# Kernel tuning notes

Hardware: AMD Instinct MI355X
Metric: run time of the kernel (lower is better)

## Reference

```python
import jax, jax.numpy as jnp
import numpy as np
from jax import lax

B, H, W = 512, 128, 128
ARCH = [1, 4096, 4096, 4096, 4096]
CONV_THRESH = 0.0
GRAPH_THRESH = 0.8
EMBED_DIM = 1


def setup_inputs() -> dict:
    key = jax.random.key(0)
    ks = jax.random.split(key, 16)
    inp = {
        "x": jax.random.normal(ks[0], (B, 1, H, W), dtype=jnp.float32),
        "conv_w": jax.random.normal(ks[1], (1, 1, 2, 2), dtype=jnp.float32) * 0.5,
        "conv_b": jax.random.normal(ks[2], (1,), dtype=jnp.float32) * 0.1,
        "rotation": jax.random.normal(ks[3], (EMBED_DIM, EMBED_DIM), dtype=jnp.float32),
        "entangle": jax.random.normal(ks[4], (EMBED_DIM, EMBED_DIM), dtype=jnp.float32),
    }
    # Linear params, torch convention W: [out_f, in_f]
    for i, (fi, fo) in enumerate(zip(ARCH[:-1], ARCH[1:])):
        inp[f"W{i+1}"] = jax.random.normal(ks[5 + 2 * i], (fo, fi), dtype=jnp.float32) / np.sqrt(fi)
        inp[f"b{i+1}"] = jax.random.normal(ks[6 + 2 * i], (fo,), dtype=jnp.float32) * 0.01
    return inp


def _forward(x, conv_w, conv_b, rotation, entangle, W1, b1, W2, b2, W3, b3, W4, b4):
    # ConvFilter: 2x2 valid conv, sigmoid(logits - thresh), mean over C,H,W -> [B]
    logits = lax.conv_general_dilated(
        x, conv_w, window_strides=(1, 1), padding="VALID",
        dimension_numbers=("NCHW", "OIHW", "NCHW"))
    logits = logits + conv_b.reshape(1, -1, 1, 1)
    conv_out = jax.nn.sigmoid(logits - CONV_THRESH).mean(axis=(1, 2, 3))  # [B]
    conv_vec = conv_out[:, None]  # [B, 1] -> embed_dim forced to 1

    # ClassicalSelfAttention (embed_dim = 1)
    q = conv_vec @ rotation                      # [B, 1]
    k = conv_vec @ entangle                      # [B, 1]
    scores = jax.nn.softmax((q @ k.T) / np.sqrt(EMBED_DIM).astype(np.float32), axis=-1)  # [B, B]
    attn_out = scores @ conv_vec                 # [B, 1]

    # tanh MLP stack
    out = attn_out
    acts = []
    for Wl, bl in ((W1, b1), (W2, b2), (W3, b3), (W4, b4)):
        out = jnp.tanh(out @ Wl.T + bl)          # [B, out_f]
        acts.append(out)

    # Vectorized fidelity adjacency over equal-shaped layer activations:
    # normalized Gram matrix squared, thresholded (replaces the O(L^2)
    # Python loop with .item() syncs in the source).
    S = jnp.stack([a.reshape(-1) for a in acts])                  # [L, B*4096]
    S_hat = S / (jnp.linalg.norm(S, axis=1, keepdims=True) + 1e-12)
    fid = (S_hat @ S_hat.T) ** 2                                   # [L, L]
    L = len(acts)
    weights = jnp.where(fid >= GRAPH_THRESH, 1.0, 0.0) * (1.0 - jnp.eye(L, dtype=fid.dtype))
    return out, weights


def reference(x, conv_w, conv_b, rotation, entangle, W1, b1, W2, b2, W3, b3, W4, b4):
    return _forward(x, conv_w, conv_b, rotation, entangle, W1, b1, W2, b2, W3, b3, W4, b4)
```

## Files before the change

kernel.cpp:

```cpp
#include <hip/hip_runtime.h>
#include <cmath>


#define NEL (512 * 4096)

typedef float  floatx4 __attribute__((ext_vector_type(4)));
typedef _Float16 halfx8 __attribute__((ext_vector_type(8)));
typedef _Float16 halfx4 __attribute__((ext_vector_type(4)));

__global__ __launch_bounds__(256) void conv_mean_kernel(
    const float* __restrict__ x, const float* __restrict__ cw,
    const float* __restrict__ cb, float* __restrict__ c_out)
{
  __shared__ float sbuf[4];
  const int b = blockIdx.x;
  const float w00 = cw[0], w01 = cw[1], w10 = cw[2], w11 = cw[3];
  const float bias = cb[0];
  const float* xb = x + (size_t)b * 128 * 128;
  float acc = 0.f;
  for (int t = threadIdx.x; t < 127 * 32; t += 256) {
    const int i  = t >> 5;
    const int j0 = (t & 31) << 2;
    const float* pr0 = xb + i * 128 + j0;
    const float* pr1 = pr0 + 128;
    const float4 a4 = *reinterpret_cast<const float4*>(pr0);
    const float  a5 = pr0[4];
    const float4 b4 = *reinterpret_cast<const float4*>(pr1);
    const float  b5 = pr1[4];
    const float a[5] = {a4.x, a4.y, a4.z, a4.w, a5};
    const float bb[5] = {b4.x, b4.y, b4.z, b4.w, b5};
    #pragma unroll
    for (int m = 0; m < 4; ++m) {
      if (j0 + m < 127) {
        float v = w00 * a[m] + w01 * a[m + 1] + w10 * bb[m] + w11 * bb[m + 1] + bias;
        acc += 1.0f / (1.0f + __expf(-v));
      }
    }
  }
  #pragma unroll
  for (int off = 32; off > 0; off >>= 1) acc += __shfl_down(acc, off, 64);
  const int lane = threadIdx.x & 63, wv = threadIdx.x >> 6;
  if (lane == 0) sbuf[wv] = acc;
  __syncthreads();
  if (threadIdx.x == 0)
    c_out[b] = (sbuf[0] + sbuf[1] + sbuf[2] + sbuf[3]) * (1.0f / 16129.0f);
}

__global__ __launch_bounds__(64) void attn_kernel(
    const float* __restrict__ c, const float* __restrict__ rot,
    const float* __restrict__ ent, float* __restrict__ attn)
{
  const int i = blockIdx.x;
  const int lane = threadIdx.x;
  const float t = rot[0] * ent[0] * c[i];
  float vals[8], cj[8];
  float mx = -1e30f;
  #pragma unroll
  for (int u = 0; u < 8; ++u) {
    float cv = c[lane + u * 64];
    cj[u] = cv;
    vals[u] = t * cv;
    mx = fmaxf(mx, vals[u]);
  }
  #pragma unroll
  for (int off = 32; off > 0; off >>= 1) mx = fmaxf(mx, __shfl_down(mx, off, 64));
  mx = __shfl(mx, 0, 64);
  float se = 0.f, sw = 0.f;
  #pragma unroll
  for (int u = 0; u < 8; ++u) {
    float e = __expf(vals[u] - mx);
    se += e;
    sw += e * cj[u];
  }
  #pragma unroll
  for (int off = 32; off > 0; off >>= 1) {
    se += __shfl_down(se, off, 64);
    sw += __shfl_down(sw, off, 64);
  }
  if (lane == 0) attn[i] = sw / se;
}

__global__ __launch_bounds__(256) void layer1_kernel(
    const float* __restrict__ attn, const float* __restrict__ W1,
    const float* __restrict__ b1, float* __restrict__ act1,
    _Float16* __restrict__ act1h)
{
  const int o = blockIdx.x * 256 + threadIdx.x;
  const int i = blockIdx.y;
  const float v = tanhf(attn[i] * W1[o] + b1[o]);
  act1[(size_t)i * 4096 + o] = v;
  if (act1h) act1h[(size_t)i * 4096 + o] = (_Float16)v;
}

#define BM 128
#define BN 128
#define BK 32
#define LDK 40

template<bool AHALF, bool FUSE>
__global__ __launch_bounds__(256, 4) void gemm_tanh_kernel(
    const void* __restrict__ Av, const float* __restrict__ W,
    const float* __restrict__ bias, float* __restrict__ C)
{
  __shared__ _Float16 As[2][BM][LDK];
  __shared__ _Float16 Ws[2][BN][LDK];
  const int K = 4096, N = 4096;
  const int tid  = threadIdx.x;
  const int lane = tid & 63;
  const int wave = tid >> 6;
  const int wm = (wave >> 1) * 64;
  const int wn = (wave & 1) * 64;
  const int q  = lane >> 4;
  const int ml = lane & 15;
  const int tileM = blockIdx.y * BM;
  const int tileN = blockIdx.x * BN;
  const int Kslice = K / gridDim.z;
  const int kbeg = blockIdx.z * Kslice;
  const int kend = kbeg + Kslice;
  float* Cb = FUSE ? C : C + (size_t)blockIdx.z * NEL;

  floatx4 acc[4][4] = {};

  const int rw  = tid >> 2;
  const int cw0 = (tid & 3) << 3;
  const int ra = tid >> 1;
  const int ca = (tid & 1) << 4;

  float4 pw[4];
  halfx8 pah[2];
  float4 paf[4];

  auto load_tile = [&](int k0) {
    if (AHALF) {
      const _Float16* Ah = (const _Float16*)Av;
      const _Float16* ap = Ah + (size_t)(tileM + ra) * K + k0 + ca;
      pah[0] = *reinterpret_cast<const halfx8*>(ap);
      pah[1] = *reinterpret_cast<const halfx8*>(ap + 8);
    } else {
      const float* Af = (const float*)Av;
      #pragma unroll
      for (int u = 0; u < 2; ++u) {
        const float* ap = Af + (size_t)(tileM + rw + u * 64) * K + k0 + cw0;
        paf[2 * u]     = *reinterpret_cast<const float4*>(ap);
        paf[2 * u + 1] = *reinterpret_cast<const float4*>(ap + 4);
      }
    }
    #pragma unroll
    for (int u = 0; u < 2; ++u) {
      const float* wp = W + (size_t)(tileN + rw + u * 64) * K + k0 + cw0;
      pw[2 * u]     = *reinterpret_cast<const float4*>(wp);
      pw[2 * u + 1] = *reinterpret_cast<const float4*>(wp + 4);
    }
  };
  auto store_tile = [&](int buf) {
    if (AHALF) {
      *reinterpret_cast<halfx8*>(&As[buf][ra][ca])     = pah[0];
      *reinterpret_cast<halfx8*>(&As[buf][ra][ca + 8]) = pah[1];
    } else {
      #pragma unroll
      for (int u = 0; u < 2; ++u) {
        halfx8 ha = { (_Float16)paf[2*u].x, (_Float16)paf[2*u].y,
                      (_Float16)paf[2*u].z, (_Float16)paf[2*u].w,
                      (_Float16)paf[2*u+1].x, (_Float16)paf[2*u+1].y,
                      (_Float16)paf[2*u+1].z, (_Float16)paf[2*u+1].w };
        *reinterpret_cast<halfx8*>(&As[buf][rw + u * 64][cw0]) = ha;
      }
    }
    #pragma unroll
    for (int u = 0; u < 2; ++u) {
      halfx8 hw = { (_Float16)pw[2*u].x, (_Float16)pw[2*u].y,
                    (_Float16)pw[2*u].z, (_Float16)pw[2*u].w,
                    (_Float16)pw[2*u+1].x, (_Float16)pw[2*u+1].y,
                    (_Float16)pw[2*u+1].z, (_Float16)pw[2*u+1].w };
      *reinterpret_cast<halfx8*>(&Ws[buf][rw + u * 64][cw0]) = hw;
    }
  };

  load_tile(kbeg);
  store_tile(0);
  int cur = 0;

  for (int k0 = kbeg; k0 < kend; k0 += BK) {
    const bool more = (k0 + BK < kend);
    __syncthreads();
    if (more) load_tile(k0 + BK);

    halfx8 af[4], bf[4];
    #pragma unroll
    for (int i = 0; i < 4; ++i)
      af[i] = *reinterpret_cast<const halfx8*>(&As[cur][wm + i * 16 + ml][q * 8]);
    #pragma unroll
    for (int j = 0; j < 4; ++j)
      bf[j] = *reinterpret_cast<const halfx8*>(&Ws[cur][wn + j * 16 + ml][q * 8]);

    #pragma unroll
    for (int i = 0; i < 4; ++i)
      #pragma unroll
      for (int j = 0; j < 4; ++j)
        acc[i][j] = __builtin_amdgcn_mfma_f32_16x16x32_f16(af[i], bf[j], acc[i][j], 0, 0, 0);

    if (more) store_tile(cur ^ 1);
    cur ^= 1;
  }

  #pragma unroll
  for (int i = 0; i < 4; ++i) {
    const int row0 = tileM + wm + i * 16 + q * 4;
    #pragma unroll
    for (int j = 0; j < 4; ++j) {
      const int col = tileN + wn + j * 16 + ml;
      if (FUSE) {
        const float bv = bias[col];
        #pragma unroll
        for (int r = 0; r < 4; ++r)
          Cb[(size_t)(row0 + r) * N + col] = tanhf(acc[i][j][r] + bv);
      } else {
        #pragma unroll
        for (int r = 0; r < 4; ++r)
          Cb[(size_t)(row0 + r) * N + col] = acc[i][j][r];
      }
    }
  }
}

template<int S, bool WRITEH>
__global__ __launch_bounds__(256) void combine_tanh_kernel(
    const float* __restrict__ part, const float* __restrict__ bias,
    float* __restrict__ outp, _Float16* __restrict__ outh)
{
  const int i4 = blockIdx.x * 256 + threadIdx.x;
  const floatx4* p4 = (const floatx4*)part;
  floatx4 s = p4[i4];
  #pragma unroll
  for (int z = 1; z < S; ++z) s += p4[(size_t)z * (NEL / 4) + i4];
  const floatx4 bv = ((const floatx4*)bias)[i4 & 1023];
  floatx4 o;
  #pragma unroll
  for (int r = 0; r < 4; ++r) o[r] = tanhf(s[r] + bv[r]);
  ((floatx4*)outp)[i4] = o;
  if (WRITEH) {
    halfx4 h = { (_Float16)o[0], (_Float16)o[1], (_Float16)o[2], (_Float16)o[3] };
    ((halfx4*)outh)[i4] = h;
  }
}

__global__ __launch_bounds__(256) void fid_dots_kernel(
    const float* __restrict__ a1, const float* __restrict__ a2,
    const float* __restrict__ a3, const float* __restrict__ a4,
    float* __restrict__ D)
{
  __shared__ float sred[4][10];
  float s[10] = {0, 0, 0, 0, 0, 0, 0, 0, 0, 0};
  const int n4 = NEL / 4;
  const int stride = gridDim.x * blockDim.x;
  const floatx4* p1 = (const floatx4*)a1;
  const floatx4* p2 = (const floatx4*)a2;
  const floatx4* p3 = (const floatx4*)a3;
  const floatx4* p4 = (const floatx4*)a4;
  for (int i = blockIdx.x * 256 + threadIdx.x; i < n4; i += stride) {
    floatx4 v1 = p1[i], v2 = p2[i], v3 = p3[i], v4 = p4[i];
    #pragma unroll
    for (int r = 0; r < 4; ++r) {
      s[0] += v1[r] * v1[r]; s[1] += v1[r] * v2[r]; s[2] += v1[r] * v3[r];
      s[3] += v1[r] * v4[r]; s[4] += v2[r] * v2[r]; s[5] += v2[r] * v3[r];
      s[6] += v2[r] * v4[r]; s[7] += v3[r] * v3[r]; s[8] += v3[r] * v4[r];
      s[9] += v4[r] * v4[r];
    }
  }
  const int lane = threadIdx.x & 63, wv = threadIdx.x >> 6;
  #pragma unroll
  for (int p = 0; p < 10; ++p) {
    float v = s[p];
    #pragma unroll
    for (int off = 32; off > 0; off >>= 1) v += __shfl_down(v, off, 64);
    if (lane == 0) sred[wv][p] = v;
  }
  __syncthreads();
  if (threadIdx.x < 10) {
    float v = sred[0][threadIdx.x] + sred[1][threadIdx.x] +
              sred[2][threadIdx.x] + sred[3][threadIdx.x];
    atomicAdd(&D[threadIdx.x * 16], v);
  }
}

__global__ void finalize_kernel(const float* __restrict__ D, float* __restrict__ wout)
{
  const int i = threadIdx.x;
  if (i >= 16) return;
  const int p = i >> 2, qq = i & 3;
  const int a = p < qq ? p : qq;
  const int b = p < qq ? qq : p;
  const int base[4] = {0, 4, 7, 9};
  const float dpq = D[(base[a] + (b - a)) * 16];
  const float npv = sqrtf(D[base[p] * 16]) + 1e-12f;
  const float nqv = sqrtf(D[base[qq] * 16]) + 1e-12f;
  const float ch = dpq / (npv * nqv);
  const float fid = ch * ch;
  wout[i] = (fid >= 0.8f && p != qq) ? 1.0f : 0.0f;
}

extern "C" void kernel_launch(void* const* d_in, const int* in_sizes, int n_in,
                              void* d_out, int out_size, void* d_ws, size_t ws_size,
                              hipStream_t stream)
{
  const float* x   = (const float*)d_in[0];
  const float* cw  = (const float*)d_in[1];
  const float* cb  = (const float*)d_in[2];
  const float* rot = (const float*)d_in[3];
  const float* ent = (const float*)d_in[4];
  const float* W1  = (const float*)d_in[5];
  const float* b1  = (const float*)d_in[6];
  const float* W2  = (const float*)d_in[7];
  const float* b2  = (const float*)d_in[8];
  const float* W3  = (const float*)d_in[9];
  const float* b3  = (const float*)d_in[10];
  const float* W4  = (const float*)d_in[11];
  const float* b4  = (const float*)d_in[12];
  float* out = (float*)d_out;

  char*  ws    = (char*)d_ws;
  float* c_buf = (float*)(ws + 0);
  float* attn  = (float*)(ws + 2048);
  float* D     = (float*)(ws + 4096);
  float* act1  = (float*)(ws + 8192);
  float* act2  = act1 + NEL;
  float* act3  = act2 + NEL;
  float* part  = act3 + NEL;
  _Float16* act1h = (_Float16*)(part + (size_t)8 * NEL);
  _Float16* act2h = act1h + NEL;
  _Float16* act3h = act2h + NEL;
  float* wout  = out + NEL;

  const size_t base_need = 8192 + (size_t)3 * NEL * 4;
  const bool sk8h = ws_size >= base_need + (size_t)8 * NEL * 4 + (size_t)3 * NEL * 2;
  const bool sk8  = ws_size >= base_need + (size_t)8 * NEL * 4;

  hipMemsetAsync(D, 0, 10 * 16 * sizeof(float), stream);
  conv_mean_kernel<<<512, 256, 0, stream>>>(x, cw, cb, c_buf);
  attn_kernel<<<512, 64, 0, stream>>>(c_buf, rot, ent, attn);
  layer1_kernel<<<dim3(16, 512), 256, 0, stream>>>(attn, W1, b1, act1,
                                                   sk8h ? act1h : nullptr);

  const int cgrid = NEL / 4 / 256;
  dim3 g8(4096 / BN, 512 / BM, 8);
  if (sk8h) {
    gemm_tanh_kernel<true,false><<<g8, 256, 0, stream>>>(act1h, W2, nullptr, part);
    combine_tanh_kernel<8,true><<<cgrid, 256, 0, stream>>>(part, b2, act2, act2h);
    gemm_tanh_kernel<true,false><<<g8, 256, 0, stream>>>(act2h, W3, nullptr, part);
    combine_tanh_kernel<8,true><<<cgrid, 256, 0, stream>>>(part, b3, act3, act3h);
    gemm_tanh_kernel<true,false><<<g8, 256, 0, stream>>>(act3h, W4, nullptr, part);
    combine_tanh_kernel<8,false><<<cgrid, 256, 0, stream>>>(part, b4, out, nullptr);
  } else if (sk8) {
    gemm_tanh_kernel<false,false><<<g8, 256, 0, stream>>>(act1, W2, nullptr, part);
    combine_tanh_kernel<8,false><<<cgrid, 256, 0, stream>>>(part, b2, act2, nullptr);
    gemm_tanh_kernel<false,false><<<g8, 256, 0, stream>>>(act2, W3, nullptr, part);
    combine_tanh_kernel<8,false><<<cgrid, 256, 0, stream>>>(part, b3, act3, nullptr);
    gemm_tanh_kernel<false,false><<<g8, 256, 0, stream>>>(act3, W4, nullptr, part);
    combine_tanh_kernel<8,false><<<cgrid, 256, 0, stream>>>(part, b4, out, nullptr);
  } else {
    dim3 g1(4096 / BN, 512 / BM, 1);
    gemm_tanh_kernel<false,true><<<g1, 256, 0, stream>>>(act1, W2, b2, act2);
    gemm_tanh_kernel<false,true><<<g1, 256, 0, stream>>>(act2, W3, b3, act3);
    gemm_tanh_kernel<false,true><<<g1, 256, 0, stream>>>(act3, W4, b4, out);
  }

  fid_dots_kernel<<<256, 256, 0, stream>>>(act1, act2, act3, out, D);
  finalize_kernel<<<1, 64, 0, stream>>>(D, wout);
}
```

Before: 434.8 us.

## Drop LDS staging in split-K GEMM, load MFMA fragments directly from global

The GEMM no longer stages tiles in shared memory. Each wave loads its own A and W fragments straight from global memory into registers, prefetching the next W slice one step ahead, and there are no __syncthreads barriers. The grid becomes 1-D with z placed as the fastest index, so the eight K-slices of one output tile are adjacent, and occupancy is lowered to 3 blocks per SM. This removes LDS traffic and barrier cost but drops cross-wave reuse: each W and A element is now fetched by two waves, which raises global and L2 traffic. The fidelity-dot kernel grid is also doubled.

```diff
diff --git a/kernel.cpp b/kernel.cpp
--- a/kernel.cpp
+++ b/kernel.cpp
@@ -92,115 +92,83 @@
   if (act1h) act1h[(size_t)i * 4096 + o] = (_Float16)v;
 }
 
-#define BM 128
-#define BN 128
-#define BK 32
-#define LDK 40
-
 template<bool AHALF, bool FUSE>
-__global__ __launch_bounds__(256, 4) void gemm_tanh_kernel(
+__global__ __launch_bounds__(256, 3) void gemm_sk_kernel(
     const void* __restrict__ Av, const float* __restrict__ W,
-    const float* __restrict__ bias, float* __restrict__ C)
-{
-  __shared__ _Float16 As[2][BM][LDK];
-  __shared__ _Float16 Ws[2][BN][LDK];
+    const float* __restrict__ bias, float* __restrict__ outp)
+{
   const int K = 4096, N = 4096;
-  const int tid  = threadIdx.x;
-  const int lane = tid & 63;
-  const int wave = tid >> 6;
-  const int wm = (wave >> 1) * 64;
-  const int wn = (wave & 1) * 64;
-  const int q  = lane >> 4;
-  const int ml = lane & 15;
-  const int tileM = blockIdx.y * BM;
-  const int tileN = blockIdx.x * BN;
-  const int Kslice = K / gridDim.z;
-  const int kbeg = blockIdx.z * Kslice;
-  const int kend = kbeg + Kslice;
-  float* Cb = FUSE ? C : C + (size_t)blockIdx.z * NEL;
+  const int id = blockIdx.x;
+  int y, x, z, kbeg, kend;
+  if (FUSE) { y = id >> 5; x = id & 31; z = 0; kbeg = 0; kend = K; }
+  else      { y = id >> 8; x = (id >> 3) & 31; z = id & 7;
+              kbeg = z * 512; kend = kbeg + 512; }
+  const int tid = threadIdx.x, lane = tid & 63, wave = tid >> 6;
+  const int wm = (wave >> 1) * 64, wn = (wave & 1) * 64;
+  const int q = lane >> 4, ml = lane & 15;
+  const int tileM = y * 128, tileN = x * 128;
+  float* Cb = FUSE ? outp : outp + (size_t)z * NEL;
+
+  const float* wRow = W + (size_t)(tileN + wn + ml) * K + q * 8;
 
   floatx4 acc[4][4] = {};
-
-  const int rw  = tid >> 2;
-  const int cw0 = (tid & 3) << 3;
-  const int ra = tid >> 1;
-  const int ca = (tid & 1) << 4;
-
-  float4 pw[4];
-  halfx8 pah[2];
-  float4 paf[4];
-
-  auto load_tile = [&](int k0) {
+  halfx8 af[4], wf[4];
+  float4 wr[8];
+
+  auto loadW = [&](float4* d, int k0) {
+    #pragma unroll
+    for (int j = 0; j < 4; ++j) {
+      const float* p = wRow + (size_t)j * 16 * K + k0;
+      d[2 * j]     = *reinterpret_cast<const float4*>(p);
+      d[2 * j + 1] = *reinterpret_cast<const float4*>(p + 4);
+    }
+  };
+  auto cvtW = [&](halfx8* h, const float4* r) {
+    #pragma unroll
+    for (int j = 0; j < 4; ++j)
+      h[j] = halfx8{ (_Float16)r[2*j].x,   (_Float16)r[2*j].y,
+                     (_Float16)r[2*j].z,   (_Float16)r[2*j].w,
+                     (_Float16)r[2*j+1].x, (_Float16)r[2*j+1].y,
+                     (_Float16)r[2*j+1].z, (_Float16)r[2*j+1].w };
+  };
+
+  const _Float16* aRowH = nullptr;
+  const float*    aRowF = nullptr;
+  if (AHALF) aRowH = (const _Float16*)Av + (size_t)(tileM + wm + ml) * K + q * 8;
+  else       aRowF = (const float*)Av    + (size_t)(tileM + wm + ml) * K + q * 8;
+
+  auto loadA = [&](halfx8* d, int k0) {
     if (AHALF) {
-      const _Float16* Ah = (const _Float16*)Av;
-      const _Float16* ap = Ah + (size_t)(tileM + ra) * K + k0 + ca;
-      pah[0] = *reinterpret_cast<const halfx8*>(ap);
-      pah[1] = *reinterpret_cast<const halfx8*>(ap + 8);
-    } else {
-      const float* Af = (const float*)Av;
       #pragma unroll
-      for (int u = 0; u < 2; ++u) {
-        const float* ap = Af + (size_t)(tileM + rw + u * 64) * K + k0 + cw0;
-        paf[2 * u]     = *reinterpret_cast<const float4*>(ap);
-        paf[2 * u + 1] = *reinterpret_cast<const float4*>(ap + 4);
-      }
-    }
-    #pragma unroll
-    for (int u = 0; u < 2; ++u) {
-      const float* wp = W + (size_t)(tileN + rw + u * 64) * K + k0 + cw0;
-      pw[2 * u]     = *reinterpret_cast<const float4*>(wp);
-      pw[2 * u + 1] = *reinterpret_cast<const float4*>(wp + 4);
-    }
-  };
-  auto store_tile = [&](int buf) {
-    if (AHALF) {
-      *reinterpret_cast<halfx8*>(&As[buf][ra][ca])     = pah[0];
-      *reinterpret_cast<halfx8*>(&As[buf][ra][ca + 8]) = pah[1];
+      for (int i = 0; i < 4; ++i)
+        d[i] = *reinterpret_cast<const halfx8*>(aRowH + (size_t)i * 16 * K + k0);
     } else {
       #pragma unroll
-      for (int u = 0; u < 2; ++u) {
-        halfx8 ha = { (_Float16)paf[2*u].x, (_Float16)paf[2*u].y,
-                      (_Float16)paf[2*u].z, (_Float16)paf[2*u].w,
-                      (_Float16)paf[2*u+1].x, (_Float16)paf[2*u+1].y,
-                      (_Float16)paf[2*u+1].z, (_Float16)paf[2*u+1].w };
-        *reinterpret_cast<halfx8*>(&As[buf][rw + u * 64][cw0]) = ha;
+      for (int i = 0; i < 4; ++i) {
+        const float* p = aRowF + (size_t)i * 16 * K + k0;
+        const float4 r0 = *reinterpret_cast<const float4*>(p);
+        const float4 r1 = *reinterpret_cast<const float4*>(p + 4);
+        d[i] = halfx8{ (_Float16)r0.x, (_Float16)r0.y, (_Float16)r0.z, (_Float16)r0.w,
+                       (_Float16)r1.x, (_Float16)r1.y, (_Float16)r1.z, (_Float16)r1.w };
       }
     }
-    #pragma unroll
-    for (int u = 0; u < 2; ++u) {
-      halfx8 hw = { (_Float16)pw[2*u].x, (_Float16)pw[2*u].y,
-                    (_Float16)pw[2*u].z, (_Float16)pw[2*u].w,
-                    (_Float16)pw[2*u+1].x, (_Float16)pw[2*u+1].y,
-                    (_Float16)pw[2*u+1].z, (_Float16)pw[2*u+1].w };
-      *reinterpret_cast<halfx8*>(&Ws[buf][rw + u * 64][cw0]) = hw;
-    }
   };
 
-  load_tile(kbeg);
-  store_tile(0);
-  int cur = 0;
-
-  for (int k0 = kbeg; k0 < kend; k0 += BK) {
-    const bool more = (k0 + BK < kend);
-    __syncthreads();
-    if (more) load_tile(k0 + BK);
-
-    halfx8 af[4], bf[4];
-    #pragma unroll
-    for (int i = 0; i < 4; ++i)
-      af[i] = *reinterpret_cast<const halfx8*>(&As[cur][wm + i * 16 + ml][q * 8]);
-    #pragma unroll
-    for (int j = 0; j < 4; ++j)
-      bf[j] = *reinterpret_cast<const halfx8*>(&Ws[cur][wn + j * 16 + ml][q * 8]);
+  loadW(wr, kbeg);
+  cvtW(wf, wr);
+
+  for (int k0 = kbeg; k0 < kend; k0 += 32) {
+    const bool more = (k0 + 32 < kend);
+    loadA(af, k0);
+    if (more) loadW(wr, k0 + 32);
 
     #pragma unroll
     for (int i = 0; i < 4; ++i)
       #pragma unroll
       for (int j = 0; j < 4; ++j)
-        acc[i][j] = __builtin_amdgcn_mfma_f32_16x16x32_f16(af[i], bf[j], acc[i][j], 0, 0, 0);
-
-    if (more) store_tile(cur ^ 1);
-    cur ^= 1;
+        acc[i][j] = __builtin_amdgcn_mfma_f32_16x16x32_f16(af[i], wf[j], acc[i][j], 0, 0, 0);
+
+    if (more) cvtW(wf, wr);
   }
 
   #pragma unroll
@@ -223,7 +191,7 @@
   }
 }
 
-template<int S, bool WRITEH>
+template<bool WRITEH>
 __global__ __launch_bounds__(256) void combine_tanh_kernel(
     const float* __restrict__ part, const float* __restrict__ bias,
     float* __restrict__ outp, _Float16* __restrict__ outh)
@@ -232,7 +200,7 @@
   const floatx4* p4 = (const floatx4*)part;
   floatx4 s = p4[i4];
   #pragma unroll
-  for (int z = 1; z < S; ++z) s += p4[(size_t)z * (NEL / 4) + i4];
+  for (int zz = 1; zz < 8; ++zz) s += p4[(size_t)zz * (NEL / 4) + i4];
   const floatx4 bv = ((const floatx4*)bias)[i4 & 1023];
   floatx4 o;
   #pragma unroll
@@ -331,39 +299,30 @@
   _Float16* act3h = act2h + NEL;
   float* wout  = out + NEL;
 
-  const size_t base_need = 8192 + (size_t)3 * NEL * 4;
-  const bool sk8h = ws_size >= base_need + (size_t)8 * NEL * 4 + (size_t)3 * NEL * 2;
-  const bool sk8  = ws_size >= base_need + (size_t)8 * NEL * 4;
+  const size_t need = 8192 + (size_t)3 * NEL * 4 + (size_t)8 * NEL * 4
+                    + (size_t)3 * NEL * 2;
+  const bool sk = ws_size >= need;
 
   hipMemsetAsync(D, 0, 10 * 16 * sizeof(float), stream);
   conv_mean_kernel<<<512, 256, 0, stream>>>(x, cw, cb, c_buf);
   attn_kernel<<<512, 64, 0, stream>>>(c_buf, rot, ent, attn);
   layer1_kernel<<<dim3(16, 512), 256, 0, stream>>>(attn, W1, b1, act1,
-                                                   sk8h ? act1h : nullptr);
+                                                   sk ? act1h : nullptr);
 
   const int cgrid = NEL / 4 / 256;
-  dim3 g8(4096 / BN, 512 / BM, 8);
-  if (sk8h) {
-    gemm_tanh_kernel<true,false><<<g8, 256, 0, stream>>>(act1h, W2, nullptr, part);
-    combine_tanh_kernel<8,true><<<cgrid, 256, 0, stream>>>(part, b2, act2, act2h);
-    gemm_tanh_kernel<true,false><<<g8, 256, 0, stream>>>(act2h, W3, nullptr, part);
-    combine_tanh_kernel<8,true><<<cgrid, 256, 0, stream>>>(part, b3, act3, act3h);
-    gemm_tanh_kernel<true,false><<<g8, 256, 0, stream>>>(act3h, W4, nullptr, part);
-    combine_tanh_kernel<8,false><<<cgrid, 256, 0, stream>>>(part, b4, out, nullptr);
-  } else if (sk8) {
-    gemm_tanh_kernel<false,false><<<g8, 256, 0, stream>>>(act1, W2, nullptr, part);
-    combine_tanh_kernel<8,false><<<cgrid, 256, 0, stream>>>(part, b2, act2, nullptr);
-    gemm_tanh_kernel<false,false><<<g8, 256, 0, stream>>>(act2, W3, nullptr, part);
-    combine_tanh_kernel<8,false><<<cgrid, 256, 0, stream>>>(part, b3, act3, nullptr);
-    gemm_tanh_kernel<false,false><<<g8, 256, 0, stream>>>(act3, W4, nullptr, part);
-    combine_tanh_kernel<8,false><<<cgrid, 256, 0, stream>>>(part, b4, out, nullptr);
+  if (sk) {
+    gemm_sk_kernel<true,false><<<1024, 256, 0, stream>>>(act1h, W2, nullptr, part);
+    combine_tanh_kernel<true><<<cgrid, 256, 0, stream>>>(part, b2, act2, act2h);
+    gemm_sk_kernel<true,false><<<1024, 256, 0, stream>>>(act2h, W3, nullptr, part);
+    combine_tanh_kernel<true><<<cgrid, 256, 0, stream>>>(part, b3, act3, act3h);
+    gemm_sk_kernel<true,false><<<1024, 256, 0, stream>>>(act3h, W4, nullptr, part);
+    combine_tanh_kernel<false><<<cgrid, 256, 0, stream>>>(part, b4, out, nullptr);
   } else {
-    dim3 g1(4096 / BN, 512 / BM, 1);
-    gemm_tanh_kernel<false,true><<<g1, 256, 0, stream>>>(act1, W2, b2, act2);
-    gemm_tanh_kernel<false,true><<<g1, 256, 0, stream>>>(act2, W3, b3, act3);
-    gemm_tanh_kernel<false,true><<<g1, 256, 0, stream>>>(act3, W4, b4, out);
-  }
-
-  fid_dots_kernel<<<256, 256, 0, stream>>>(act1, act2, act3, out, D);
+    gemm_sk_kernel<false,true><<<128, 256, 0, stream>>>(act1, W2, b2, act2);
+    gemm_sk_kernel<false,true><<<128, 256, 0, stream>>>(act2, W3, b3, act3);
+    gemm_sk_kernel<false,true><<<128, 256, 0, stream>>>(act3, W4, b4, out);
+  }
+
+  fid_dots_kernel<<<512, 256, 0, stream>>>(act1, act2, act3, out, D);
   finalize_kernel<<<1, 64, 0, stream>>>(D, wout);
 }
```

After: 545.3 us. 25.4% more time.
